# Optimization experiments

Measured on AMD Instinct MI355X. Metric: run time of the kernel, lower is better.

Reference implementation:

```python
import jax, jax.numpy as jnp
import numpy as np

NUM_LABELS = 1024
NUM_CAMS = 8


def setup_inputs() -> dict:
    key = jax.random.key(0)
    k1, k2, k3 = jax.random.split(key, 3)
    feats = jax.random.normal(k1, (16384, 2048), dtype=jnp.float32)
    labels = jax.random.randint(k2, (16384,), 0, NUM_LABELS, dtype=jnp.int64)
    cam_ids = jax.random.randint(k3, (16384,), 0, NUM_CAMS, dtype=jnp.int64)
    return {"feats": feats, "labels": labels, "cam_ids": cam_ids}


def reference(feats, labels, cam_ids):
    # Combined (person-id, camera-id) segment id -> fused segment-mean.
    seg = labels * NUM_CAMS + cam_ids  # [N]
    num_segments = NUM_LABELS * NUM_CAMS
    sums = jax.ops.segment_sum(feats, seg, num_segments=num_segments)  # [S, D]
    counts = jax.ops.segment_sum(jnp.ones_like(seg, dtype=feats.dtype), seg,
                                 num_segments=num_segments)  # [S]
    means = sums / jnp.maximum(counts, 1.0)[:, None]
    # targets[i] = mean of feats over group(label_i, cam_i); detached in torch.
    targets = jax.lax.stop_gradient(means[seg])  # [N, D]
    # SmoothL1 (beta=1), reduction='mean'
    d = feats - targets
    ad = jnp.abs(d)
    loss = jnp.mean(jnp.where(ad < 1.0, 0.5 * d * d, ad - 0.5))
    return loss
```

## Files before the change

kernel.cpp:

```cpp
#include <hip/hip_runtime.h>
#include <hip/hip_bf16.h>

#define N_ROWS 16384
#define D_COLS 2048
#define NUM_LABELS 1024
#define NUM_CAMS 8
#define NUM_SEG (NUM_LABELS * NUM_CAMS)
#define MAXPER 64
#define R_REG 12
#define F4_PER_ROW (D_COLS / 4)
#define NUM_BLOCKS (NUM_SEG * 2)

__global__ void build_lists_kernel(const int* __restrict__ labels,
                                   const int* __restrict__ cams,
                                   int* __restrict__ counts,
                                   int* __restrict__ lists) {
    int i = blockIdx.x * blockDim.x + threadIdx.x;
    if (i < N_ROWS) {
        int seg = labels[i] * NUM_CAMS + cams[i];
        int pos = atomicAdd(&counts[seg], 1);
        if (pos < MAXPER) lists[seg * MAXPER + pos] = i;
    }
}

__device__ __forceinline__ float smooth_l1(float d) {
    float ad = fabsf(d);
    return ad < 1.0f ? 0.5f * d * d : ad - 0.5f;
}

__global__ __launch_bounds__(256) void seg_loss_kernel(const float* __restrict__ feats,
                                                       const int* __restrict__ counts,
                                                       const int* __restrict__ lists,
                                                       float* __restrict__ partials) {
    int bid  = blockIdx.x;
    int seg  = bid >> 1;
    int half = bid & 1;
    int tid  = threadIdx.x;

    __shared__ int slist[R_REG];

    int cnt = counts[seg];
    if (tid < R_REG && tid < cnt)
        slist[tid] = lists[seg * MAXPER + tid];
    __syncthreads();

    int rows = cnt < R_REG ? cnt : R_REG;

    const float4* base = (const float4*)feats + (half * 256 + tid);

    float4 v[R_REG];
#pragma unroll
    for (int r = 0; r < R_REG; ++r) {
        v[r] = make_float4(0.f, 0.f, 0.f, 0.f);
        if (r < rows)
            v[r] = base[(size_t)slist[r] * F4_PER_ROW];
    }

    float mx = 0.f, my = 0.f, mz = 0.f, mw = 0.f;
#pragma unroll
    for (int r = 0; r < R_REG; ++r) {
        mx += v[r].x; my += v[r].y; mz += v[r].z; mw += v[r].w;
    }
    for (int r = R_REG; r < cnt && r < MAXPER; ++r) {
        float4 a = base[(size_t)lists[seg * MAXPER + r] * F4_PER_ROW];
        mx += a.x; my += a.y; mz += a.z; mw += a.w;
    }

    float inv = 1.0f / (float)(cnt > 0 ? cnt : 1);
    mx *= inv; my *= inv; mz *= inv; mw *= inv;

    float loss = 0.0f;
#pragma unroll
    for (int r = 0; r < R_REG; ++r) {
        float w = (r < rows) ? 1.0f : 0.0f;
        loss += w * (smooth_l1(v[r].x - mx) + smooth_l1(v[r].y - my)
                   + smooth_l1(v[r].z - mz) + smooth_l1(v[r].w - mw));
    }
    for (int r = R_REG; r < cnt && r < MAXPER; ++r) {
        float4 a = base[(size_t)lists[seg * MAXPER + r] * F4_PER_ROW];
        loss += smooth_l1(a.x - mx) + smooth_l1(a.y - my)
              + smooth_l1(a.z - mz) + smooth_l1(a.w - mw);
    }

    for (int o = 32; o > 0; o >>= 1)
        loss += __shfl_down(loss, o, 64);

    __shared__ float wsum[4];
    int lane = tid & 63;
    int wid  = tid >> 6;
    if (lane == 0) wsum[wid] = loss;
    __syncthreads();
    if (tid == 0)
        partials[bid] = wsum[0] + wsum[1] + wsum[2] + wsum[3];
}

__global__ __launch_bounds__(256) void reduce_kernel(const float* __restrict__ partials,
                                                     float* __restrict__ out) {
    int tid = threadIdx.x;
    float s = 0.0f;
    for (int i = tid; i < NUM_BLOCKS; i += 256)
        s += partials[i];

    for (int o = 32; o > 0; o >>= 1)
        s += __shfl_down(s, o, 64);

    __shared__ float wsum[4];
    int lane = tid & 63;
    int wid  = tid >> 6;
    if (lane == 0) wsum[wid] = s;
    __syncthreads();
    if (tid == 0)
        out[0] = (wsum[0] + wsum[1] + wsum[2] + wsum[3])
               * (1.0f / ((float)N_ROWS * (float)D_COLS));
}

extern "C" void kernel_launch(void* const* d_in, const int* in_sizes, int n_in,
                              void* d_out, int out_size, void* d_ws, size_t ws_size,
                              hipStream_t stream) {
    const float* feats = (const float*)d_in[0];
    const int* labels  = (const int*)d_in[1];
    const int* cams    = (const int*)d_in[2];
    float* out = (float*)d_out;

    int* counts     = (int*)d_ws;
    int* lists      = counts + NUM_SEG;
    float* partials = (float*)(lists + NUM_SEG * MAXPER);

    hipMemsetAsync(counts, 0, NUM_SEG * sizeof(int), stream);

    build_lists_kernel<<<(N_ROWS + 255) / 256, 256, 0, stream>>>(labels, cams, counts, lists);
    seg_loss_kernel<<<NUM_BLOCKS, 256, 0, stream>>>(feats, counts, lists, partials);
    reduce_kernel<<<1, 256, 0, stream>>>(partials, out);
}
```

Before: 217.6 us.

## Process eight segments per block to amortize per-block overhead

Each block now loops over a group of eight segments instead of handling one, which shrinks the grid eightfold. Counts and the first twelve indices for all eight segments are staged in LDS with one load phase and one sync. The register row cache shrinks from twelve to eight float4 and the launch bounds request higher occupancy. The trade-off is less memory parallelism per block, because segments are processed serially inside the loop.

```diff
diff --git a/kernel.cpp b/kernel.cpp
--- a/kernel.cpp
+++ b/kernel.cpp
@@ -7,9 +7,12 @@
 #define NUM_CAMS 8
 #define NUM_SEG (NUM_LABELS * NUM_CAMS)
 #define MAXPER 64
-#define R_REG 12
+#define GSEG 8
+#define NUM_GROUPS (NUM_SEG / GSEG)
+#define NUM_BLOCKS (NUM_GROUPS * 2)
+#define FAST_R 8
+#define IDX_LDS 12
 #define F4_PER_ROW (D_COLS / 4)
-#define NUM_BLOCKS (NUM_SEG * 2)
 
 __global__ void build_lists_kernel(const int* __restrict__ labels,
                                    const int* __restrict__ cams,
@@ -28,64 +31,89 @@
     return ad < 1.0f ? 0.5f * d * d : ad - 0.5f;
 }
 
-__global__ __launch_bounds__(256) void seg_loss_kernel(const float* __restrict__ feats,
-                                                       const int* __restrict__ counts,
-                                                       const int* __restrict__ lists,
-                                                       float* __restrict__ partials) {
+__global__ __launch_bounds__(256, 8) void group_loss_kernel(const float* __restrict__ feats,
+                                                            const int* __restrict__ counts,
+                                                            const int* __restrict__ lists,
+                                                            float* __restrict__ partials) {
     int bid  = blockIdx.x;
-    int seg  = bid >> 1;
+    int grp  = bid >> 1;
     int half = bid & 1;
     int tid  = threadIdx.x;
+    int seg0 = grp * GSEG;
 
-    __shared__ int slist[R_REG];
+    __shared__ int   scnt[GSEG];
+    __shared__ int   sidx[GSEG][IDX_LDS];
+    __shared__ float wsum[4];
 
-    int cnt = counts[seg];
-    if (tid < R_REG && tid < cnt)
-        slist[tid] = lists[seg * MAXPER + tid];
+    if (tid < GSEG) {
+        scnt[tid] = counts[seg0 + tid];
+    } else if (tid < GSEG + GSEG * IDX_LDS) {
+        int j = tid - GSEG;
+        int s = j / IDX_LDS;
+        int r = j - s * IDX_LDS;
+        sidx[s][r] = lists[(seg0 + s) * MAXPER + r];
+    }
     __syncthreads();
 
-    int rows = cnt < R_REG ? cnt : R_REG;
+    const float4* base = (const float4*)feats + (half * 256 + tid);
+    float loss = 0.0f;
 
-    const float4* base = (const float4*)feats + (half * 256 + tid);
+#pragma unroll 1
+    for (int s = 0; s < GSEG; ++s) {
+        int cnt  = scnt[s];
+        int rows = cnt < FAST_R ? cnt : FAST_R;
 
-    float4 v[R_REG];
+        float4 v[FAST_R];
 #pragma unroll
-    for (int r = 0; r < R_REG; ++r) {
-        v[r] = make_float4(0.f, 0.f, 0.f, 0.f);
-        if (r < rows)
-            v[r] = base[(size_t)slist[r] * F4_PER_ROW];
-    }
+        for (int r = 0; r < FAST_R; ++r) {
+            v[r] = make_float4(0.f, 0.f, 0.f, 0.f);
+            if (r < rows)
+                v[r] = base[(size_t)sidx[s][r] * F4_PER_ROW];
+        }
 
-    float mx = 0.f, my = 0.f, mz = 0.f, mw = 0.f;
+        float mx = 0.f, my = 0.f, mz = 0.f, mw = 0.f;
 #pragma unroll
-    for (int r = 0; r < R_REG; ++r) {
-        mx += v[r].x; my += v[r].y; mz += v[r].z; mw += v[r].w;
-    }
-    for (int r = R_REG; r < cnt && r < MAXPER; ++r) {
-        float4 a = base[(size_t)lists[seg * MAXPER + r] * F4_PER_ROW];
-        mx += a.x; my += a.y; mz += a.z; mw += a.w;
-    }
+        for (int r = 0; r < FAST_R; ++r) {
+            mx += v[r].x; my += v[r].y; mz += v[r].z; mw += v[r].w;
+        }
 
-    float inv = 1.0f / (float)(cnt > 0 ? cnt : 1);
-    mx *= inv; my *= inv; mz *= inv; mw *= inv;
+        if (cnt > FAST_R) {
+            for (int r = FAST_R; r < cnt && r < IDX_LDS; ++r) {
+                float4 a = base[(size_t)sidx[s][r] * F4_PER_ROW];
+                mx += a.x; my += a.y; mz += a.z; mw += a.w;
+            }
+            for (int r = IDX_LDS; r < cnt && r < MAXPER; ++r) {
+                float4 a = base[(size_t)lists[(seg0 + s) * MAXPER + r] * F4_PER_ROW];
+                mx += a.x; my += a.y; mz += a.z; mw += a.w;
+            }
+        }
 
-    float loss = 0.0f;
+        float inv = 1.0f / (float)(cnt > 0 ? cnt : 1);
+        mx *= inv; my *= inv; mz *= inv; mw *= inv;
+
 #pragma unroll
-    for (int r = 0; r < R_REG; ++r) {
-        float w = (r < rows) ? 1.0f : 0.0f;
-        loss += w * (smooth_l1(v[r].x - mx) + smooth_l1(v[r].y - my)
-                   + smooth_l1(v[r].z - mz) + smooth_l1(v[r].w - mw));
-    }
-    for (int r = R_REG; r < cnt && r < MAXPER; ++r) {
-        float4 a = base[(size_t)lists[seg * MAXPER + r] * F4_PER_ROW];
-        loss += smooth_l1(a.x - mx) + smooth_l1(a.y - my)
-              + smooth_l1(a.z - mz) + smooth_l1(a.w - mw);
+        for (int r = 0; r < FAST_R; ++r) {
+            if (r < rows)
+                loss += smooth_l1(v[r].x - mx) + smooth_l1(v[r].y - my)
+                      + smooth_l1(v[r].z - mz) + smooth_l1(v[r].w - mw);
+        }
+        if (cnt > FAST_R) {
+            for (int r = FAST_R; r < cnt && r < IDX_LDS; ++r) {
+                float4 a = base[(size_t)sidx[s][r] * F4_PER_ROW];
+                loss += smooth_l1(a.x - mx) + smooth_l1(a.y - my)
+                      + smooth_l1(a.z - mz) + smooth_l1(a.w - mw);
+            }
+            for (int r = IDX_LDS; r < cnt && r < MAXPER; ++r) {
+                float4 a = base[(size_t)lists[(seg0 + s) * MAXPER + r] * F4_PER_ROW];
+                loss += smooth_l1(a.x - mx) + smooth_l1(a.y - my)
+                      + smooth_l1(a.z - mz) + smooth_l1(a.w - mw);
+            }
+        }
     }
 
     for (int o = 32; o > 0; o >>= 1)
         loss += __shfl_down(loss, o, 64);
 
-    __shared__ float wsum[4];
     int lane = tid & 63;
     int wid  = tid >> 6;
     if (lane == 0) wsum[wid] = loss;
@@ -129,6 +157,6 @@
     hipMemsetAsync(counts, 0, NUM_SEG * sizeof(int), stream);
 
     build_lists_kernel<<<(N_ROWS + 255) / 256, 256, 0, stream>>>(labels, cams, counts, lists);
-    seg_loss_kernel<<<NUM_BLOCKS, 256, 0, stream>>>(feats, counts, lists, partials);
+    group_loss_kernel<<<NUM_BLOCKS, 256, 0, stream>>>(feats, counts, lists, partials);
     reduce_kernel<<<1, 256, 0, stream>>>(partials, out);
 }
```

After: 204.9 us. 5.8% less time.
